# Kernel tuning notes

Hardware: AMD Instinct MI355X
Metric: run time of the kernel (lower is better)

Reference implementation:

```python
import jax, jax.numpy as jnp
import numpy as np

N_QUBITS = 4
N_LAYERS = 3
LETTERS = "ijkl"  # one axis label per qubit; batch axis is 'b'
CNOT = np.array([[1, 0, 0, 0], [0, 1, 0, 0], [0, 0, 0, 1], [0, 0, 1, 0]], dtype=np.complex64).reshape(2, 2, 2, 2)


def _apply_1q(state, U, w, batched):
    # state: [B,2,2,2,2]; U: [2,2] (shared) or [B,2,2] (per-sample)
    s = "b" + LETTERS
    t = LETTERS[w]
    u = ("b" if batched else "") + "z" + t
    return jnp.einsum(f"{u},{s}->{s.replace(t, 'z')}", U, state)


def _apply_cnot(state, c, t):
    s = "b" + LETTERS
    a, b = LETTERS[c], LETTERS[t]
    out = s.replace(a, "x").replace(b, "y")
    return jnp.einsum(f"xy{a}{b},{s}->{out}", jnp.asarray(CNOT), state)


def _rx(theta):
    # theta: [B] -> batched RX gates [B,2,2]
    c = jnp.cos(theta / 2).astype(jnp.complex64)
    s = (-1j * jnp.sin(theta / 2)).astype(jnp.complex64)
    return jnp.stack([jnp.stack([c, s], -1), jnp.stack([s, c], -1)], -2)


def _rz(a):
    e = jnp.exp(-1j * a.astype(jnp.complex64) / 2)
    zero = jnp.zeros((), jnp.complex64)
    return jnp.array([[e, zero], [zero, jnp.conj(e)]])


def _ry(a):
    c = jnp.cos(a / 2).astype(jnp.complex64)
    s = jnp.sin(a / 2).astype(jnp.complex64)
    return jnp.array([[c, -s], [s, c]])


def _rot(phi, theta, omega):
    # PennyLane Rot = RZ(omega) @ RY(theta) @ RZ(phi)
    return _rz(omega) @ _ry(theta) @ _rz(phi)


def _circuit(qparams, z):
    # qparams: [n_layers, n_qubits, 3] float32; z: [B, n_qubits] float32
    B = z.shape[0]
    state = jnp.zeros((B,) + (2,) * N_QUBITS, jnp.complex64)
    state = state.at[:, 0, 0, 0, 0].set(1.0 + 0.0j)
    # data-encoding RX layer (per-sample angles -> batched gates)
    for w in range(N_QUBITS):
        state = _apply_1q(state, _rx(z[:, w]), w, batched=True)
    # variational layers: Rot on every wire then CNOT ladder
    for layer in range(N_LAYERS):
        for w in range(N_QUBITS):
            U = _rot(qparams[layer, w, 0], qparams[layer, w, 1], qparams[layer, w, 2])
            state = _apply_1q(state, U, w, batched=False)
        for w in range(N_QUBITS - 1):
            state = _apply_cnot(state, w, w + 1)
    probs = jnp.abs(state) ** 2  # [B,2,2,2,2] float32
    zsign = jnp.array([1.0, -1.0], jnp.float32)
    s = "b" + LETTERS
    evs = [jnp.einsum(f"{s},{LETTERS[w]}->b", probs, zsign) for w in range(N_QUBITS)]
    return jnp.stack(evs, axis=-1)  # [B, n_qubits]


def reference(x, enc_w, enc_b, qparams, cls_w, cls_b, bn_gamma, bn_beta):
    B = x.shape[0]
    # avg_pool2d(kernel_size=6) on 28x28 -> 4x4 (floor division drops last 4 rows/cols)
    pooled = x[:, :, :24, :24].reshape(B, 1, 4, 6, 4, 6).mean(axis=(3, 5)).reshape(B, 16)
    z = pooled @ enc_w.T + enc_b  # [B, n_qubits]
    evs = _circuit(qparams, z)    # [B, n_qubits]
    out = evs @ cls_w.T + cls_b   # [B, output_dim]
    # BatchNorm1d in training mode: biased batch statistics, eps=1e-5
    mu = out.mean(axis=0)
    var = ((out - mu) ** 2).mean(axis=0)
    out = (out - mu) / jnp.sqrt(var + 1e-5) * bn_gamma + bn_beta
    return out


def setup_inputs() -> dict:
    key = jax.random.key(0)
    ks = jax.random.split(key, 6)
    B = 32768
    return {
        "x": jax.random.normal(ks[0], (B, 1, 28, 28), jnp.float32),
        "enc_w": jax.random.normal(ks[1], (N_QUBITS, 16), jnp.float32) * 0.25,
        "enc_b": jnp.zeros((N_QUBITS,), jnp.float32),
        "qparams": jax.random.normal(ks[2], (N_LAYERS, N_QUBITS, 3), jnp.float32),
        "cls_w": jax.random.normal(ks[3], (4, N_QUBITS), jnp.float32) * 0.5,
        "cls_b": jnp.zeros((4,), jnp.float32),
        "bn_gamma": jnp.ones((4,), jnp.float32),
        "bn_beta": jnp.zeros((4,), jnp.float32),
    }
```

## Files before the change

kernel.cpp:

```cpp
#include <hip/hip_runtime.h>
#include <math.h>


#define BTOT 32768
#define SPB  16
#define NBLK (BTOT / SPB)
#define SSTR 576

__device__ float g_partials[NBLK * 8];

__global__ __launch_bounds__(256) void fused_kernel(
    const float* __restrict__ x,
    const float* __restrict__ enc_w, const float* __restrict__ enc_b,
    const float* __restrict__ qparams, const float* __restrict__ cls_w,
    const float* __restrict__ cls_b,
    float* __restrict__ preBN)
{
    __shared__ __align__(16) float sx[SPB * SSTR];
    __shared__ float sVr[16 * 17];
    __shared__ float sVi[16 * 17];
    __shared__ float sW2[4 * 17];
    __shared__ float red[4][8];

    const int tid = threadIdx.x;
    const int s0  = blockIdx.x * SPB;
    const float4* xb = (const float4*)x;

    float4 st[9];
    #pragma unroll
    for (int it = 0; it < 9; ++it) {
        const int gid  = it * 256 + tid;
        const int c    = gid / 144;
        const int o    = gid - c * 144;
        const int row  = o / 6;
        const int col4 = o - row * 6;
        st[it] = xb[(size_t)(s0 + c) * 196 + row * 7 + col4];
    }

    if (tid < 64) {
        {
            int j = tid >> 4, i = tid & 15;
            float acc = 0.f;
            #pragma unroll
            for (int w = 0; w < 4; ++w)
                acc += cls_w[j * 4 + w] * ((i & (8 >> w)) ? -1.f : 1.f);
            sW2[j * 17 + i] = acc;
        }
        if (tid < 16) {
            const int t = tid;
            float pr[16], pi[16];
            #pragma unroll
            for (int i = 0; i < 16; ++i) { pr[i] = (i == t) ? 1.f : 0.f; pi[i] = 0.f; }
            #pragma unroll
            for (int layer = 0; layer < 3; ++layer) {
                #pragma unroll
                for (int w = 0; w < 4; ++w) {
                    const float* qp = qparams + (layer * 4 + w) * 3;
                    float phi = qp[0], th = qp[1], om = qp[2];
                    float c, sn, ca, sa, cd, sd;
                    __sincosf(0.5f * th, &sn, &c);
                    __sincosf(0.5f * (phi + om), &sa, &ca);
                    __sincosf(0.5f * (phi - om), &sd, &cd);
                    float u00r =  c * ca, u00i = -c * sa;
                    float u01r = -sn * cd, u01i = -sn * sd;
                    float u10r =  sn * cd, u10i = -sn * sd;
                    float u11r =  c * ca, u11i =  c * sa;
                    const int m = 8 >> w;
                    #pragma unroll
                    for (int idx = 0; idx < 16; ++idx) {
                        if (idx & m) continue;
                        const int i1 = idx | m;
                        float ar = pr[idx], ai = pi[idx], br = pr[i1], bi = pi[i1];
                        pr[idx] = u00r*ar - u00i*ai + u01r*br - u01i*bi;
                        pi[idx] = u00r*ai + u00i*ar + u01r*bi + u01i*br;
                        pr[i1]  = u10r*ar - u10i*ai + u11r*br - u11i*bi;
                        pi[i1]  = u10r*ai + u10i*ar + u11r*bi + u11i*br;
                    }
                }
                #pragma unroll
                for (int w = 0; w < 3; ++w) {
                    const int mc = 8 >> w, mt = 8 >> (w + 1);
                    #pragma unroll
                    for (int idx = 0; idx < 16; ++idx) {
                        if ((idx & mc) && !(idx & mt)) {
                            const int i1 = idx | mt;
                            float tr = pr[idx], ti = pi[idx];
                            pr[idx] = pr[i1]; pi[idx] = pi[i1];
                            pr[i1] = tr;      pi[i1] = ti;
                        }
                    }
                }
            }
            const int p = __popc(t) & 3;
            #pragma unroll
            for (int i = 0; i < 16; ++i) {
                float re = pr[i], im = pi[i], vr, vi;
                if (p == 0)      { vr = re;  vi = im;  }
                else if (p == 1) { vr = im;  vi = -re; }
                else if (p == 2) { vr = -re; vi = -im; }
                else             { vr = -im; vi = re;  }
                sVr[i * 17 + t] = vr;
                sVi[i * 17 + t] = vi;
            }
        }
    }

    #pragma unroll
    for (int it = 0; it < 9; ++it)
        ((float4*)sx)[it * 256 + tid] = st[it];

    __syncthreads();

    const int s = tid >> 4, cell = tid & 15;
    const int cr = cell >> 2, cc = cell & 3;
    int srot = s;
    srot -= (srot >= 12) ? 12 : ((srot >= 6) ? 6 : 0);
    const float* sb = &sx[s * SSTR + cr * 6 * 24 + cc * 6];
    float sum = 0.f;
    #pragma unroll
    for (int rr = 0; rr < 6; ++rr) {
        int r = rr + srot; r -= (r >= 6) ? 6 : 0;
        const float2* rp = (const float2*)(sb + r * 24);
        float2 a = rp[0], b = rp[1], c2 = rp[2];
        sum += (a.x + a.y) + (b.x + b.y) + (c2.x + c2.y);
    }
    const float pv = sum * (1.f / 36.f);

    float z[4];
    #pragma unroll
    for (int j = 0; j < 4; ++j) z[j] = enc_w[j * 16 + cell] * pv;
    #pragma unroll
    for (int m = 1; m <= 8; m <<= 1) {
        #pragma unroll
        for (int j = 0; j < 4; ++j) z[j] += __shfl_xor(z[j], m, 64);
    }
    #pragma unroll
    for (int j = 0; j < 4; ++j) z[j] += enc_b[j];

    float cz[4], sz[4];
    #pragma unroll
    for (int j = 0; j < 4; ++j) __sincosf(0.5f * z[j], &sz[j], &cz[j]);
    float a01[4] = {cz[0]*cz[1], cz[0]*sz[1], sz[0]*cz[1], sz[0]*sz[1]};
    float a23[4] = {cz[2]*cz[3], cz[2]*sz[3], sz[2]*cz[3], sz[2]*sz[3]};
    float rv[16];
    #pragma unroll
    for (int k = 0; k < 16; ++k) rv[k] = a01[k >> 2] * a23[k & 3];

    float ar = 0.f, ai = 0.f;
    #pragma unroll
    for (int k = 0; k < 16; ++k) {
        ar += sVr[cell * 17 + k] * rv[k];
        ai += sVi[cell * 17 + k] * rv[k];
    }
    const float prob = ar * ar + ai * ai;
    float out[4];
    #pragma unroll
    for (int j = 0; j < 4; ++j) out[j] = sW2[j * 17 + cell] * prob;
    #pragma unroll
    for (int m = 1; m <= 8; m <<= 1) {
        #pragma unroll
        for (int j = 0; j < 4; ++j) out[j] += __shfl_xor(out[j], m, 64);
    }
    #pragma unroll
    for (int j = 0; j < 4; ++j) out[j] += cls_b[j];

    if (cell == 0)
        ((float4*)preBN)[s0 + s] = make_float4(out[0], out[1], out[2], out[3]);

    const float w = (cell == 0) ? 1.f : 0.f;
    float v8[8] = {out[0]*w, out[1]*w, out[2]*w, out[3]*w,
                   out[0]*out[0]*w, out[1]*out[1]*w, out[2]*out[2]*w, out[3]*out[3]*w};
    #pragma unroll
    for (int m = 0; m < 8; ++m) {
        v8[m] += __shfl_down(v8[m], 32, 64);
        v8[m] += __shfl_down(v8[m], 16, 64);
    }
    const int wave = tid >> 6, lane = tid & 63;
    if (lane == 0) {
        #pragma unroll
        for (int m = 0; m < 8; ++m) red[wave][m] = v8[m];
    }
    __syncthreads();
    if (tid < 8)
        g_partials[blockIdx.x * 8 + tid] =
            red[0][tid] + red[1][tid] + red[2][tid] + red[3][tid];
}

__global__ __launch_bounds__(256) void bn_kernel(
    const float* __restrict__ gamma, const float* __restrict__ beta,
    float* __restrict__ out)
{
    const int tid = threadIdx.x;
    float acc[8] = {0, 0, 0, 0, 0, 0, 0, 0};
    const float4* p4 = (const float4*)g_partials;
    #pragma unroll
    for (int it = 0; it < NBLK / 256; ++it) {
        int b = it * 256 + tid;
        float4 a = p4[b * 2], c = p4[b * 2 + 1];
        acc[0] += a.x; acc[1] += a.y; acc[2] += a.z; acc[3] += a.w;
        acc[4] += c.x; acc[5] += c.y; acc[6] += c.z; acc[7] += c.w;
    }
    #pragma unroll
    for (int off = 32; off >= 1; off >>= 1) {
        #pragma unroll
        for (int m = 0; m < 8; ++m) acc[m] += __shfl_xor(acc[m], off, 64);
    }
    __shared__ float red[4][8];
    const int wave = tid >> 6, lane = tid & 63;
    if (lane == 0) {
        #pragma unroll
        for (int m = 0; m < 8; ++m) red[wave][m] = acc[m];
    }
    __syncthreads();
    float sums[8];
    #pragma unroll
    for (int m = 0; m < 8; ++m)
        sums[m] = red[0][m] + red[1][m] + red[2][m] + red[3][m];

    const int s = blockIdx.x * 256 + tid;
    const float invB = 1.f / (float)BTOT;
    float4 v = ((const float4*)out)[s];
    float o[4] = {v.x, v.y, v.z, v.w};
    #pragma unroll
    for (int j = 0; j < 4; ++j) {
        float mu   = sums[j] * invB;
        float var  = sums[4 + j] * invB - mu * mu;
        float rstd = rsqrtf(var + 1e-5f);
        o[j] = (o[j] - mu) * rstd * gamma[j] + beta[j];
    }
    ((float4*)out)[s] = make_float4(o[0], o[1], o[2], o[3]);
}

extern "C" void kernel_launch(void* const* d_in, const int* in_sizes, int n_in,
                              void* d_out, int out_size, void* d_ws, size_t ws_size,
                              hipStream_t stream)
{
    const float* x        = (const float*)d_in[0];
    const float* enc_w    = (const float*)d_in[1];
    const float* enc_b    = (const float*)d_in[2];
    const float* qparams  = (const float*)d_in[3];
    const float* cls_w    = (const float*)d_in[4];
    const float* cls_b    = (const float*)d_in[5];
    const float* bn_gamma = (const float*)d_in[6];
    const float* bn_beta  = (const float*)d_in[7];

    float* outp = (float*)d_out;
    (void)d_ws; (void)ws_size;

    fused_kernel<<<NBLK, 256, 0, stream>>>(x, enc_w, enc_b, qparams, cls_w,
                                           cls_b, outp);
    bn_kernel<<<128, 256, 0, stream>>>(bn_gamma, bn_beta, outp);
}
```

Before: 176.5 us.

## Split fused kernel into prep, pooling, and quantum-circuit kernels

Moves the per-block circuit unitary and classifier-sign precomputation into a single one-block prep kernel, and splits pooling from the circuit evaluation. Pooled features go through a global buffer, and the circuit kernel reloads the precomputed matrices into shared memory. This removes the redundant 16-thread unitary simulation that every block ran serially before its barrier. In exchange it adds two kernel launches and a global round trip of the pooled data.

```diff
diff --git a/kernel.cpp b/kernel.cpp
--- a/kernel.cpp
+++ b/kernel.cpp
@@ -7,20 +7,83 @@
 #define NBLK (BTOT / SPB)
 #define SSTR 576
 
+__device__ float g_prep[576];
+__device__ float g_pooled[BTOT * 16];
 __device__ float g_partials[NBLK * 8];
 
-__global__ __launch_bounds__(256) void fused_kernel(
-    const float* __restrict__ x,
-    const float* __restrict__ enc_w, const float* __restrict__ enc_b,
-    const float* __restrict__ qparams, const float* __restrict__ cls_w,
-    const float* __restrict__ cls_b,
-    float* __restrict__ preBN)
+__global__ __launch_bounds__(64) void prep_kernel(
+    const float* __restrict__ qparams, const float* __restrict__ cls_w)
+{
+    const int t = threadIdx.x;
+    {
+        int j = t >> 4, i = t & 15;
+        float acc = 0.f;
+        #pragma unroll
+        for (int w = 0; w < 4; ++w)
+            acc += cls_w[j * 4 + w] * ((i & (8 >> w)) ? -1.f : 1.f);
+        g_prep[512 + j * 16 + i] = acc;
+    }
+    if (t < 16) {
+        float pr[16], pi[16];
+        #pragma unroll
+        for (int i = 0; i < 16; ++i) { pr[i] = (i == t) ? 1.f : 0.f; pi[i] = 0.f; }
+        #pragma unroll
+        for (int layer = 0; layer < 3; ++layer) {
+            #pragma unroll
+            for (int w = 0; w < 4; ++w) {
+                const float* qp = qparams + (layer * 4 + w) * 3;
+                float phi = qp[0], th = qp[1], om = qp[2];
+                float c, s, ca, sa, cd, sd;
+                __sincosf(0.5f * th, &s, &c);
+                __sincosf(0.5f * (phi + om), &sa, &ca);
+                __sincosf(0.5f * (phi - om), &sd, &cd);
+                float u00r =  c * ca, u00i = -c * sa;
+                float u01r = -s * cd, u01i = -s * sd;
+                float u10r =  s * cd, u10i = -s * sd;
+                float u11r =  c * ca, u11i =  c * sa;
+                const int m = 8 >> w;
+                #pragma unroll
+                for (int idx = 0; idx < 16; ++idx) {
+                    if (idx & m) continue;
+                    const int i1 = idx | m;
+                    float ar = pr[idx], ai = pi[idx], br = pr[i1], bi = pi[i1];
+                    pr[idx] = u00r*ar - u00i*ai + u01r*br - u01i*bi;
+                    pi[idx] = u00r*ai + u00i*ar + u01r*bi + u01i*br;
+                    pr[i1]  = u10r*ar - u10i*ai + u11r*br - u11i*bi;
+                    pi[i1]  = u10r*ai + u10i*ar + u11r*bi + u11i*br;
+                }
+            }
+            #pragma unroll
+            for (int w = 0; w < 3; ++w) {
+                const int mc = 8 >> w, mt = 8 >> (w + 1);
+                #pragma unroll
+                for (int idx = 0; idx < 16; ++idx) {
+                    if ((idx & mc) && !(idx & mt)) {
+                        const int i1 = idx | mt;
+                        float tr = pr[idx], ti = pi[idx];
+                        pr[idx] = pr[i1]; pi[idx] = pi[i1];
+                        pr[i1] = tr;      pi[i1] = ti;
+                    }
+                }
+            }
+        }
+        const int p = __popc(t) & 3;
+        #pragma unroll
+        for (int i = 0; i < 16; ++i) {
+            float re = pr[i], im = pi[i], vr, vi;
+            if (p == 0)      { vr = re;  vi = im;  }
+            else if (p == 1) { vr = im;  vi = -re; }
+            else if (p == 2) { vr = -re; vi = -im; }
+            else             { vr = -im; vi = re;  }
+            g_prep[i * 16 + t]       = vr;
+            g_prep[256 + i * 16 + t] = vi;
+        }
+    }
+}
+
+__global__ __launch_bounds__(256) void pool_kernel(const float* __restrict__ x)
 {
     __shared__ __align__(16) float sx[SPB * SSTR];
-    __shared__ float sVr[16 * 17];
-    __shared__ float sVi[16 * 17];
-    __shared__ float sW2[4 * 17];
-    __shared__ float red[4][8];
 
     const int tid = threadIdx.x;
     const int s0  = blockIdx.x * SPB;
@@ -36,75 +99,6 @@
         const int col4 = o - row * 6;
         st[it] = xb[(size_t)(s0 + c) * 196 + row * 7 + col4];
     }
-
-    if (tid < 64) {
-        {
-            int j = tid >> 4, i = tid & 15;
-            float acc = 0.f;
-            #pragma unroll
-            for (int w = 0; w < 4; ++w)
-                acc += cls_w[j * 4 + w] * ((i & (8 >> w)) ? -1.f : 1.f);
-            sW2[j * 17 + i] = acc;
-        }
-        if (tid < 16) {
-            const int t = tid;
-            float pr[16], pi[16];
-            #pragma unroll
-            for (int i = 0; i < 16; ++i) { pr[i] = (i == t) ? 1.f : 0.f; pi[i] = 0.f; }
-            #pragma unroll
-            for (int layer = 0; layer < 3; ++layer) {
-                #pragma unroll
-                for (int w = 0; w < 4; ++w) {
-                    const float* qp = qparams + (layer * 4 + w) * 3;
-                    float phi = qp[0], th = qp[1], om = qp[2];
-                    float c, sn, ca, sa, cd, sd;
-                    __sincosf(0.5f * th, &sn, &c);
-                    __sincosf(0.5f * (phi + om), &sa, &ca);
-                    __sincosf(0.5f * (phi - om), &sd, &cd);
-                    float u00r =  c * ca, u00i = -c * sa;
-                    float u01r = -sn * cd, u01i = -sn * sd;
-                    float u10r =  sn * cd, u10i = -sn * sd;
-                    float u11r =  c * ca, u11i =  c * sa;
-                    const int m = 8 >> w;
-                    #pragma unroll
-                    for (int idx = 0; idx < 16; ++idx) {
-                        if (idx & m) continue;
-                        const int i1 = idx | m;
-                        float ar = pr[idx], ai = pi[idx], br = pr[i1], bi = pi[i1];
-                        pr[idx] = u00r*ar - u00i*ai + u01r*br - u01i*bi;
-                        pi[idx] = u00r*ai + u00i*ar + u01r*bi + u01i*br;
-                        pr[i1]  = u10r*ar - u10i*ai + u11r*br - u11i*bi;
-                        pi[i1]  = u10r*ai + u10i*ar + u11r*bi + u11i*br;
-                    }
-                }
-                #pragma unroll
-                for (int w = 0; w < 3; ++w) {
-                    const int mc = 8 >> w, mt = 8 >> (w + 1);
-                    #pragma unroll
-                    for (int idx = 0; idx < 16; ++idx) {
-                        if ((idx & mc) && !(idx & mt)) {
-                            const int i1 = idx | mt;
-                            float tr = pr[idx], ti = pi[idx];
-                            pr[idx] = pr[i1]; pi[idx] = pi[i1];
-                            pr[i1] = tr;      pi[i1] = ti;
-                        }
-                    }
-                }
-            }
-            const int p = __popc(t) & 3;
-            #pragma unroll
-            for (int i = 0; i < 16; ++i) {
-                float re = pr[i], im = pi[i], vr, vi;
-                if (p == 0)      { vr = re;  vi = im;  }
-                else if (p == 1) { vr = im;  vi = -re; }
-                else if (p == 2) { vr = -re; vi = -im; }
-                else             { vr = -im; vi = re;  }
-                sVr[i * 17 + t] = vr;
-                sVi[i * 17 + t] = vi;
-            }
-        }
-    }
-
     #pragma unroll
     for (int it = 0; it < 9; ++it)
         ((float4*)sx)[it * 256 + tid] = st[it];
@@ -124,7 +118,36 @@
         float2 a = rp[0], b = rp[1], c2 = rp[2];
         sum += (a.x + a.y) + (b.x + b.y) + (c2.x + c2.y);
     }
-    const float pv = sum * (1.f / 36.f);
+    g_pooled[(size_t)(s0 + s) * 16 + cell] = sum * (1.f / 36.f);
+}
+
+__global__ __launch_bounds__(256) void qc_kernel(
+    const float* __restrict__ enc_w, const float* __restrict__ enc_b,
+    const float* __restrict__ cls_b,
+    float* __restrict__ preBN)
+{
+    __shared__ float sVr[16 * 17];
+    __shared__ float sVi[16 * 17];
+    __shared__ float sW2[4 * 17];
+    __shared__ float red[4][8];
+
+    const int tid = threadIdx.x;
+    const int s0  = blockIdx.x * SPB;
+    const int s = tid >> 4, cell = tid & 15;
+
+    const float pv = g_pooled[(size_t)(s0 + s) * 16 + cell];
+
+    #pragma unroll
+    for (int g0 = 0; g0 < 576; g0 += 256) {
+        int g = g0 + tid;
+        if (g < 576) {
+            float v = g_prep[g];
+            int row = (g >> 4) & 15, col = g & 15;
+            if (g < 256)      sVr[row * 17 + col] = v;
+            else if (g < 512) sVi[row * 17 + col] = v;
+            else              sW2[(g - 512) / 16 * 17 + col] = v;
+        }
+    }
 
     float z[4];
     #pragma unroll
@@ -145,6 +168,8 @@
     float rv[16];
     #pragma unroll
     for (int k = 0; k < 16; ++k) rv[k] = a01[k >> 2] * a23[k & 3];
+
+    __syncthreads();
 
     float ar = 0.f, ai = 0.f;
     #pragma unroll
@@ -247,7 +272,8 @@
     float* outp = (float*)d_out;
     (void)d_ws; (void)ws_size;
 
-    fused_kernel<<<NBLK, 256, 0, stream>>>(x, enc_w, enc_b, qparams, cls_w,
-                                           cls_b, outp);
+    prep_kernel<<<1, 64, 0, stream>>>(qparams, cls_w);
+    pool_kernel<<<NBLK, 256, 0, stream>>>(x);
+    qc_kernel<<<NBLK, 256, 0, stream>>>(enc_w, enc_b, cls_b, outp);
     bn_kernel<<<128, 256, 0, stream>>>(bn_gamma, bn_beta, outp);
 }
```

After: 179.0 us. About the same (+1.4%).
